# Kernel tuning notes

Measured on AMD Instinct MI355X. Metric: run time of the kernel, lower is better.

## Reference

```python
import jax, jax.numpy as jnp
import numpy as np

T = 2048        # Tmax encoder frames
EPROJS = 1024   # encoder projection dim (Henc)
DUNITS = 512    # prediction net hidden
EMBED = 512     # embedding dim
JOINT = 512     # joint space dim
ODIM = 10000    # output vocab
BLANK = 0


def setup_inputs() -> dict:
    key = jax.random.key(0)
    ks = jax.random.split(key, 11)
    def g(k, shape, scale):
        return (jax.random.normal(k, shape, dtype=jnp.float32) * scale)
    inp = {
        'h': jax.random.normal(ks[0], (T, EPROJS), dtype=jnp.float32),
        # Embedding with padding_idx=blank -> blank row zeroed
        'embed': g(ks[1], (ODIM, EMBED), 0.05).at[BLANK].set(0.0),
        # LSTMCell params (torch gate order: i, f, g, o)
        'W_ih': g(ks[2], (4 * DUNITS, EMBED), 1.0 / np.sqrt(EMBED)),
        'W_hh': g(ks[3], (4 * DUNITS, DUNITS), 1.0 / np.sqrt(DUNITS)),
        'b_ih': g(ks[4], (4 * DUNITS,), 0.01),
        'b_hh': g(ks[5], (4 * DUNITS,), 0.01),
        # joint network
        'W_enc': g(ks[6], (JOINT, EPROJS), 1.0 / np.sqrt(EPROJS)),
        'b_enc': g(ks[7], (JOINT,), 0.01),
        'W_dec': g(ks[8], (JOINT, DUNITS), 1.0 / np.sqrt(DUNITS)),  # no bias
        'W_out': g(ks[9], (ODIM, JOINT), 1.0 / np.sqrt(JOINT)),
        'b_out': g(ks[10], (ODIM,), 0.01),
    }
    return inp


def _lstm_cell(x, h_prev, c_prev, W_ih, W_hh, b_ih, b_hh):
    gates = W_ih @ x + b_ih + W_hh @ h_prev + b_hh  # (4*DUNITS,)
    i, f, g, o = jnp.split(gates, 4)
    c = jax.nn.sigmoid(f) * c_prev + jax.nn.sigmoid(i) * jnp.tanh(g)
    h = jax.nn.sigmoid(o) * jnp.tanh(c)
    return h, c


def reference(h, embed, W_ih, W_hh, b_ih, b_hh, W_enc, b_enc, W_dec, W_out, b_out):
    # Precompute encoder-side joint projection (same math, hoisted out of loop)
    h_proj = h @ W_enc.T + b_enc  # (T, JOINT)

    # Initial prediction-net step on zero embedding from zero state
    zeros_e = jnp.zeros((EMBED,), dtype=h.dtype)
    zeros_d = jnp.zeros((DUNITS,), dtype=h.dtype)
    y0, c0 = _lstm_cell(zeros_e, zeros_d, zeros_d, W_ih, W_hh, b_ih, b_hh)

    def step(carry, hp_t):
        y, c, score = carry
        # joint: tanh(lin_enc(h_t) + lin_dec(y)) -> lin_out -> log_softmax
        ytu = jax.nn.log_softmax(W_out @ jnp.tanh(hp_t + W_dec @ y) + b_out)
        logp = jnp.max(ytu)
        pred = jnp.argmax(ytu)
        emitted = pred != BLANK
        # Candidate prediction-net update with embedded token
        ey = embed[pred]
        y_new, c_new = _lstm_cell(ey, y, c, W_ih, W_hh, b_ih, b_hh)
        y = jnp.where(emitted, y_new, y)
        c = jnp.where(emitted, c_new, c)
        score = score + jnp.where(emitted, logp, jnp.zeros_like(logp))
        tok = jnp.where(emitted, pred, BLANK).astype(jnp.int32)
        return (y, c, score), tok

    (y, c, score), yseq = jax.lax.scan(step, (y0, c0, jnp.float32(0.0)), h_proj)
    # yseq: (T,) int32, BLANK where no symbol was emitted at that frame
    return yseq, score
```

## Files before the change

kernel.cpp:

```cpp
#include <hip/hip_runtime.h>
#include <stdint.h>

typedef unsigned long long u64;
typedef uint32_t u32;

#define NB     256
#define NT     256
#define TMAX   2048
#define EPROJS 1024
#define DUNITS 512
#define EMBED  512
#define JOINT  512
#define ODIM   10000

#define N_LSTM 32
#define CONS0  32
#define N_CONS 223
#define AGG_B  255
#define MAGIC  0xD07ED07Eu

#define WS_PK   0
#define WS_SA   7168
#define WS_DN   14336
#define WS_AGG  15360
#define WS_CNT  16384
#define WS_Y    17408
#define WS_U    21504
#define WS_HP   54272

__device__ __forceinline__ float aloadf(const float* p){
  return __hip_atomic_load(p, __ATOMIC_RELAXED, __HIP_MEMORY_SCOPE_AGENT);
}
__device__ __forceinline__ void astoref(float* p, float v){
  __hip_atomic_store(p, v, __ATOMIC_RELAXED, __HIP_MEMORY_SCOPE_AGENT);
}
__device__ __forceinline__ u64 aloadu64(const u64* p){
  return __hip_atomic_load(p, __ATOMIC_RELAXED, __HIP_MEMORY_SCOPE_AGENT);
}
__device__ __forceinline__ void astoreu64(u64* p, u64 v){
  __hip_atomic_store(p, v, __ATOMIC_RELAXED, __HIP_MEMORY_SCOPE_AGENT);
}
__device__ __forceinline__ u32 aloadu32(const u32* p){
  return __hip_atomic_load(p, __ATOMIC_RELAXED, __HIP_MEMORY_SCOPE_AGENT);
}
__device__ __forceinline__ void astoreu32(u32* p, u32 v){
  __hip_atomic_store(p, v, __ATOMIC_RELAXED, __HIP_MEMORY_SCOPE_AGENT);
}

__device__ __forceinline__ u32 ordbits(float f){
  u32 u = __float_as_uint(f);
  return (u & 0x80000000u) ? ~u : (u | 0x80000000u);
}
__device__ __forceinline__ float unordbits(u32 o){
  u32 u = (o & 0x80000000u) ? (o & 0x7fffffffu) : ~o;
  return __uint_as_float(u);
}
__device__ __forceinline__ float sigmoidf_(float x){ return 1.0f/(1.0f+expf(-x)); }

__device__ __forceinline__ float wredsum(float v){
  #pragma unroll
  for (int o=32;o>0;o>>=1) v += __shfl_xor(v, o);
  return v;
}
__device__ __forceinline__ u64 wredmax64(u64 v){
  #pragma unroll
  for (int o=32;o>0;o>>=1){ u64 x = __shfl_xor(v, o); v = (x>v)?x:v; }
  return v;
}

__device__ __forceinline__ int zslot(int j){
  return (j&7)*64 + ((j>>3) ^ ((j&7)<<2));
}

#define LOAD8(dst, baseptr) { const float4* _p=(const float4*)(baseptr); \
  float4 _a=_p[0], _b=_p[1]; \
  dst[0]=_a.x; dst[1]=_a.y; dst[2]=_a.z; dst[3]=_a.w; \
  dst[4]=_b.x; dst[5]=_b.y; dst[6]=_b.z; dst[7]=_b.w; }

__global__ void rnnt_init(char* ws){
  u32* p = (u32*)ws;
  const int stride = blockDim.x * gridDim.x;
  for (int i = blockIdx.x*blockDim.x + threadIdx.x; i < 13568; i += stride) p[i] = 0u;
}

__global__ void __launch_bounds__(NT, 1)
rnnt_decode(const float* __restrict__ h,    const float* __restrict__ embed,
            const float* __restrict__ W_ih, const float* __restrict__ W_hh,
            const float* __restrict__ b_ih, const float* __restrict__ b_hh,
            const float* __restrict__ W_enc,const float* __restrict__ b_enc,
            const float* __restrict__ W_dec,const float* __restrict__ W_out,
            const float* __restrict__ b_out,
            float* __restrict__ out, char* __restrict__ ws)
{
  const int b    = blockIdx.x;
  const int tid  = threadIdx.x;
  const int lane = tid & 63;
  const int w    = tid >> 6;

  u64*   ytag = (u64*)(ws + WS_Y);
  float* ubuf = (float*)(ws + WS_U);
  u64*  pkall = (u64*)(ws + WS_PK);
  u64*  saall = (u64*)(ws + WS_SA);
  u32*  done  = (u32*)(ws + WS_DN);
  u32*  aggr  = (u32*)(ws + WS_AGG);
  u32*  cnt   = (u32*)(ws + WS_CNT);
  float* hp   = (float*)(ws + WS_HP);

  __shared__ float smem[8192];
  float* PL = smem;
  float* GL = &smem[4416];
  u64*   R64= (u64*)&smem[4480];
  float* RF = &smem[4488];
  float* YO = &smem[4492];
  float* SL = &smem[4544];

  {
    float (*lds_h)[EPROJS] = (float(*)[EPROJS])smem;
    #pragma unroll
    for (int r=0;r<8;r++){
      const float4 hv = *(const float4*)(h + (size_t)(8*b + r)*EPROJS + tid*4);
      *(float4*)&lds_h[r][tid*4] = hv;
    }
    __syncthreads();
    for (int p=0;p<2;p++){
      const int j = p*NT + tid;
      float acc[8] = {0,0,0,0,0,0,0,0};
      const float4* wrow = (const float4*)(W_enc + (size_t)j*EPROJS);
      for (int k4=0;k4<EPROJS/4;k4++){
        const float4 wv = wrow[k4];
        #pragma unroll
        for (int t8=0;t8<8;t8++){
          const float4 hv = *(const float4*)&lds_h[t8][k4*4];
          acc[t8] = fmaf(wv.x,hv.x, fmaf(wv.y,hv.y, fmaf(wv.z,hv.z, fmaf(wv.w,hv.w, acc[t8]))));
        }
      }
      const float be = b_enc[j];
      #pragma unroll
      for (int t8=0;t8<8;t8++)
        astoref(&hp[(size_t)(8*b+t8)*JOINT + j], acc[t8] + be);
    }
    asm volatile("s_waitcnt vmcnt(0)" ::: "memory");
    if (tid==0) astoreu32(&done[b], MAGIC);
    __syncthreads();
  }

  if (b < N_LSTM){
    const int d = b;
    float wih[16][8], whh[16][8];
    #pragma unroll
    for (int q=0;q<16;q++){
      const int gr = w*DUNITS + 16*d + q;
      LOAD8(wih[q], W_ih + (size_t)gr*EMBED  + lane*8);
      LOAD8(whh[q], W_hh + (size_t)gr*DUNITS + lane*8);
    }
    float wdc0[16], wdc1[16];
    {
      const float4* p0 = (const float4*)(W_dec + (size_t)(2*tid)*DUNITS   + 16*d);
      const float4* p1 = (const float4*)(W_dec + (size_t)(2*tid+1)*DUNITS + 16*d);
      #pragma unroll
      for (int k4=0;k4<4;k4++){
        const float4 a = p0[k4];
        wdc0[4*k4+0]=a.x; wdc0[4*k4+1]=a.y; wdc0[4*k4+2]=a.z; wdc0[4*k4+3]=a.w;
        const float4 c = p1[k4];
        wdc1[4*k4+0]=c.x; wdc1[4*k4+1]=c.y; wdc1[4*k4+2]=c.z; wdc1[4*k4+3]=c.w;
      }
    }
    float bias_r = 0.0f;
    if (tid < 64){
      const int gr = (tid>>4)*DUNITS + 16*d + (tid&15);
      bias_r = b_ih[gr] + b_hh[gr];
    }
    float c_st = 0.0f, y_st = 0.0f;
    if (tid < 16){
      const int j = 16*d + tid;
      const float gi = b_ih[j]            + b_hh[j];
      const float gg = b_ih[2*DUNITS + j] + b_hh[2*DUNITS + j];
      const float go = b_ih[3*DUNITS + j] + b_hh[3*DUNITS + j];
      c_st = sigmoidf_(gi)*tanhf(gg);
      y_st = sigmoidf_(go)*tanhf(c_st);
      YO[tid] = y_st;
      astoreu64(&ytag[j], ((u64)1u<<32) | (u64)__float_as_uint(y_st));
    }
    __syncthreads();
    {
      float p0=0.f, p1=0.f;
      #pragma unroll
      for (int k=0;k<16;k++){ p0 = fmaf(wdc0[k], YO[k], p0); p1 = fmaf(wdc1[k], YO[k], p1); }
      float* up = ubuf + 1*4096 + (d&7)*512;
      atomicAdd(&up[2*tid],   p0);
      atomicAdd(&up[2*tid+1], p1);
    }
    asm volatile("s_waitcnt vmcnt(0)" ::: "memory");
    __syncthreads();
    if (tid < 8) atomicAdd(&cnt[tid*32], 1u);

    for (int t=0;t<TMAX;t++){
      const u32 g = (u32)(t+1);
      u64 ya, yb;
      for(;;){
        ya = aloadu64(&ytag[2*tid]); yb = aloadu64(&ytag[2*tid+1]);
        const int ok = ((u32)(ya>>32)==g) & ((u32)(yb>>32)==g);
        if (__syncthreads_and(ok)) break;
      }
      SL[zslot(2*tid)]   = __uint_as_float((u32)ya);
      SL[zslot(2*tid+1)] = __uint_as_float((u32)yb);
      __syncthreads();
      float y8[8];
      #pragma unroll
      for (int e=0;e<8;e++) y8[e] = SL[e*64 + (lane ^ (e<<2))];
      float vp[16];
      #pragma unroll
      for (int q=0;q<16;q++){
        float a=0.f;
        #pragma unroll
        for (int k=0;k<8;k++) a = fmaf(whh[q][k], y8[k], a);
        vp[q] = a;
      }
      u64 pk = 0;
      for(;;){
        if (tid < N_CONS) pk = aloadu64(&pkall[(g&3)*224 + tid]);
        const int ok = (tid < N_CONS) ? ((u32)(pk>>48) >= g) : 1;
        if (__syncthreads_and(ok)) break;
      }
      const u64 m = wredmax64(pk);
      if (lane==0) R64[w] = m;
      const int predw = (int)((~(u32)m) & 0xFFFFu);
      float e8[8];
      LOAD8(e8, embed + (size_t)predw*EMBED + 8*lane);
      __syncthreads();
      u64 best = R64[0];
      #pragma unroll
      for (int i=1;i<4;i++){ const u64 x=R64[i]; best = (x>best)?x:best; }
      const int pred = (int)((~(u32)best) & 0xFFFFu);
      const int emitted = (pred != 0);
      if (m != best){
        LOAD8(e8, embed + (size_t)pred*EMBED + 8*lane);
      }
      if (tid < 64){
        u64* uz = (u64*)(ubuf + (g&1)*4096 + (d&7)*512) + (d>>3)*64;
        astoreu64(&uz[tid], 0ull);
      }
      #pragma unroll
      for (int q=0;q<16;q++){
        float a = vp[q];
        #pragma unroll
        for (int k=0;k<8;k++) a = fmaf(wih[q][k], e8[k], a);
        PL[(w*16+q)*68 + lane] = a;
      }
      __syncthreads();
      if (tid < 64){
        const float* row = &PL[tid*68];
        float s = bias_r;
        #pragma unroll
        for (int k4=0;k4<16;k4++){
          const float4 v4 = *(const float4*)&row[4*k4];
          s += v4.x + v4.y + v4.z + v4.w;
        }
        GL[tid] = s;
      }
      __syncthreads();
      if (tid < 16){
        const float gi=GL[tid], gf=GL[16+tid], gg=GL[32+tid], go=GL[48+tid];
        const float cn = sigmoidf_(gf)*c_st + sigmoidf_(gi)*tanhf(gg);
        const float yn = sigmoidf_(go)*tanhf(cn);
        if (emitted){ c_st = cn; y_st = yn; }
        YO[tid] = y_st;
        if (t < TMAX-1)
          astoreu64(&ytag[16*d + tid], ((u64)(g+1)<<32) | (u64)__float_as_uint(y_st));
      }
      __syncthreads();
      if (t < TMAX-1){
        float p0=0.f, p1=0.f;
        #pragma unroll
        for (int k=0;k<16;k++){ p0 = fmaf(wdc0[k], YO[k], p0); p1 = fmaf(wdc1[k], YO[k], p1); }
        float* up = ubuf + ((g+1)&1)*4096 + (d&7)*512;
        atomicAdd(&up[2*tid],   p0);
        atomicAdd(&up[2*tid+1], p1);
      }
      asm volatile("s_waitcnt vmcnt(0)" ::: "memory");
      __syncthreads();
      if (t < TMAX-1 && tid < 8) atomicAdd(&cnt[tid*32], 1u);
    }
  }
  else if (b < AGG_B){
    const int cb = b - CONS0;
    int rowstart, rowcnt;
    if (cb < 188){ rowstart = cb*45;                 rowcnt = 45; }
    else         { rowstart = 8460 + (cb-188)*44;    rowcnt = 44; }
    float wout[12][8];
    #pragma unroll
    for (int q=0;q<12;q++){
      const int s = 12*w + q;
      if (s < rowcnt){
        LOAD8(wout[q], W_out + (size_t)(rowstart+s)*JOINT + lane*8);
      } else {
        #pragma unroll
        for (int k=0;k<8;k++) wout[q][k]=0.f;
      }
    }
    float my_bo = 0.f; int my_row = 0; bool my_val = false;
    if (tid < rowcnt){ my_val = true; my_row = rowstart + tid; my_bo = b_out[my_row]; }
    const u32* agrep = &aggr[(cb&7)*32];

    for(;;){
      const int ok = (aloadu32(&done[tid]) == MAGIC);
      if (__syncthreads_and(ok)) break;
    }

    const u32* cp = &cnt[(cb&7)*32];
    const int j0 = 2*tid, j1 = 2*tid+1;
    const int s0 = zslot(j0), s1 = zslot(j1);
    for (int t=0;t<TMAX;t++){
      const u32 g = (u32)(t+1);
      const float2 h2 = *(const float2*)(hp + (size_t)t*JOINT + j0);
      if (tid==0){ while (aloadu32(cp) < 32u*g) {} }
      __syncthreads();
      float u0 = 0.f, u1 = 0.f;
      {
        const u64* ub64 = (const u64*)(ubuf + (g&1)*4096) + tid;
        u64 v[8];
        #pragma unroll
        for (int r=0;r<8;r++) v[r] = aloadu64(ub64 + r*256);
        #pragma unroll
        for (int r=0;r<8;r++){
          u0 += __uint_as_float((u32)v[r]);
          u1 += __uint_as_float((u32)(v[r]>>32));
        }
      }
      SL[s0] = tanhf(h2.x + u0);
      SL[s1] = tanhf(h2.y + u1);
      __syncthreads();
      float z8[8];
      #pragma unroll
      for (int e=0;e<8;e++) z8[e] = SL[e*64 + (lane ^ (e<<2))];
      #pragma unroll
      for (int q=0;q<12;q++){
        float a=0.f;
        #pragma unroll
        for (int k=0;k<8;k++) a = fmaf(wout[q][k], z8[k], a);
        PL[(12*w+q)*68 + lane] = a;
      }
      __syncthreads();
      u64 key = 0; float lg = 0.f;
      if (tid < 48){
        const float* row = &PL[tid*68];
        float s = my_bo;
        #pragma unroll
        for (int k4=0;k4<16;k4++){
          const float4 v4 = *(const float4*)&row[4*k4];
          s += v4.x + v4.y + v4.z + v4.w;
        }
        lg = s;
        if (my_val) key = ((u64)ordbits(lg)<<16) | (u64)(0xFFFFu & ~(u32)my_row);
      }
      if (w == 0){
        const u64 bk = wredmax64(key);
        const float mw = unordbits((u32)(bk>>16));
        const float e  = my_val ? __expf(lg - mw) : 0.f;
        const float sw = wredsum(e);
        if (lane == 0){
          while ((int)(g - aloadu32(agrep)) > 3) __builtin_amdgcn_s_sleep(2);
          astoreu64(&saall[(g&3)*224 + cb], ((u64)g<<32) | (u64)__float_as_uint(sw));
          astoreu64(&pkall[(g&3)*224 + cb], ((u64)g<<48) | bk);
        }
      }
      __syncthreads();
    }
  }
  else {
    float score = 0.0f;
    for (int t=0;t<TMAX;t++){
      const u32 g = (u32)(t+1);
      const u64* pks = pkall + (g&3)*224;
      const u64* sas = saall + (g&3)*224;
      u64 pk=0, sa=0;
      for(;;){
        if (tid < N_CONS){ pk = aloadu64(&pks[tid]); sa = aloadu64(&sas[tid]); }
        const int ok = (tid < N_CONS) ? (((u32)(pk>>48)==g) & (((u32)(sa>>32))==g)) : 1;
        if (__syncthreads_and(ok)) break;
      }
      { u64 m = wredmax64(pk); if (lane==0) R64[w]=m; }
      __syncthreads();
      u64 best = R64[0];
      #pragma unroll
      for (int i=1;i<4;i++){ const u64 x=R64[i]; best = (x>best)?x:best; }
      const float mstar = unordbits((u32)(best>>16));
      float term = (tid < N_CONS) ?
        __uint_as_float((u32)sa) * __expf(unordbits((u32)(pk>>16)) - mstar) : 0.f;
      term = wredsum(term);
      if (lane==0) RF[w] = term;
      __syncthreads();
      if (tid==0){
        const float S = RF[0]+RF[1]+RF[2]+RF[3];
        const int pred = (int)((~(u32)best) & 0xFFFFu);
        if (pred != 0) score += -logf(S);
        out[t] = (float)pred;
      }
      __syncthreads();
      if (tid < 8) astoreu32(&aggr[tid*32], g);
    }
    if (tid==0) out[TMAX] = score;
  }
}

extern "C" void kernel_launch(void* const* d_in, const int* in_sizes, int n_in,
                              void* d_out, int out_size, void* d_ws, size_t ws_size,
                              hipStream_t stream)
{
  const float* h     = (const float*)d_in[0];
  const float* embed = (const float*)d_in[1];
  const float* W_ih  = (const float*)d_in[2];
  const float* W_hh  = (const float*)d_in[3];
  const float* b_ih  = (const float*)d_in[4];
  const float* b_hh  = (const float*)d_in[5];
  const float* W_enc = (const float*)d_in[6];
  const float* b_enc = (const float*)d_in[7];
  const float* W_dec = (const float*)d_in[8];
  const float* W_out = (const float*)d_in[9];
  const float* b_out = (const float*)d_in[10];
  float* out = (float*)d_out;
  char* ws = (char*)d_ws;

  hipLaunchKernelGGL(rnnt_init, dim3(32), dim3(NT), 0, stream, ws);
  hipLaunchKernelGGL(rnnt_decode, dim3(NB), dim3(NT), 0, stream,
                     h, embed, W_ih, W_hh, b_ih, b_hh, W_enc, b_enc, W_dec, W_out, b_out,
                     out, ws);
}
```

Before: 16.71 ms.

## Replace LDS partial-sum reductions with wave shuffles and per-block done flags

Both the LSTM blocks and the joint-output consumer blocks now reduce their dot-product partials with in-wave shuffle sums instead of writing to shared memory and doing a second serial pass. The shared counter that the LSTM blocks incremented atomically is replaced by a per-block generation flag, which consumers poll in parallel with a block-wide vote. The aggregator back-pressure load is also issued early. This is meant to shorten the per-timestep critical path on the serial decode chain, at the cost of more shuffle instructions and wider polling traffic.

```diff
diff --git a/kernel.cpp b/kernel.cpp
--- a/kernel.cpp
+++ b/kernel.cpp
@@ -23,10 +23,10 @@
 #define WS_SA   7168
 #define WS_DN   14336
 #define WS_AGG  15360
-#define WS_CNT  16384
-#define WS_Y    17408
-#define WS_U    21504
-#define WS_HP   54272
+#define WS_UD   16384
+#define WS_Y    20480
+#define WS_U    24576
+#define WS_HP   57344
 
 __device__ __forceinline__ float aloadf(const float* p){
   return __hip_atomic_load(p, __ATOMIC_RELAXED, __HIP_MEMORY_SCOPE_AGENT);
@@ -80,7 +80,7 @@
 __global__ void rnnt_init(char* ws){
   u32* p = (u32*)ws;
   const int stride = blockDim.x * gridDim.x;
-  for (int i = blockIdx.x*blockDim.x + threadIdx.x; i < 13568; i += stride) p[i] = 0u;
+  for (int i = blockIdx.x*blockDim.x + threadIdx.x; i < 14336; i += stride) p[i] = 0u;
 }
 
 __global__ void __launch_bounds__(NT, 1)
@@ -103,11 +103,10 @@
   u64*  saall = (u64*)(ws + WS_SA);
   u32*  done  = (u32*)(ws + WS_DN);
   u32*  aggr  = (u32*)(ws + WS_AGG);
-  u32*  cnt   = (u32*)(ws + WS_CNT);
+  u32*  udone = (u32*)(ws + WS_UD);
   float* hp   = (float*)(ws + WS_HP);
 
   __shared__ float smem[8192];
-  float* PL = smem;
   float* GL = &smem[4416];
   u64*   R64= (u64*)&smem[4480];
   float* RF = &smem[4488];
@@ -165,10 +164,10 @@
         wdc1[4*k4+0]=c.x; wdc1[4*k4+1]=c.y; wdc1[4*k4+2]=c.z; wdc1[4*k4+3]=c.w;
       }
     }
-    float bias_r = 0.0f;
-    if (tid < 64){
-      const int gr = (tid>>4)*DUNITS + 16*d + (tid&15);
-      bias_r = b_ih[gr] + b_hh[gr];
+    float bias_l = 0.0f;
+    if (lane < 16){
+      const int gr = w*DUNITS + 16*d + lane;
+      bias_l = b_ih[gr] + b_hh[gr];
     }
     float c_st = 0.0f, y_st = 0.0f;
     if (tid < 16){
@@ -192,7 +191,7 @@
     }
     asm volatile("s_waitcnt vmcnt(0)" ::: "memory");
     __syncthreads();
-    if (tid < 8) atomicAdd(&cnt[tid*32], 1u);
+    if (tid==0) astoreu32(&udone[d*32], 1u);
 
     for (int t=0;t<TMAX;t++){
       const u32 g = (u32)(t+1);
@@ -240,23 +239,22 @@
         u64* uz = (u64*)(ubuf + (g&1)*4096 + (d&7)*512) + (d>>3)*64;
         astoreu64(&uz[tid], 0ull);
       }
-      #pragma unroll
-      for (int q=0;q<16;q++){
-        float a = vp[q];
-        #pragma unroll
-        for (int k=0;k<8;k++) a = fmaf(wih[q][k], e8[k], a);
-        PL[(w*16+q)*68 + lane] = a;
-      }
-      __syncthreads();
-      if (tid < 64){
-        const float* row = &PL[tid*68];
-        float s = bias_r;
-        #pragma unroll
-        for (int k4=0;k4<16;k4++){
-          const float4 v4 = *(const float4*)&row[4*k4];
-          s += v4.x + v4.y + v4.z + v4.w;
-        }
-        GL[tid] = s;
+      {
+        float a[16];
+        #pragma unroll
+        for (int q=0;q<16;q++){
+          float acc = vp[q];
+          #pragma unroll
+          for (int k=0;k<8;k++) acc = fmaf(wih[q][k], e8[k], acc);
+          a[q] = acc;
+        }
+        float rs = 0.f;
+        #pragma unroll
+        for (int q=0;q<16;q++){
+          const float s = wredsum(a[q]);
+          if (lane==q) rs = s;
+        }
+        if (lane < 16) GL[w*16 + lane] = rs + bias_l;
       }
       __syncthreads();
       if (tid < 16){
@@ -279,7 +277,7 @@
       }
       asm volatile("s_waitcnt vmcnt(0)" ::: "memory");
       __syncthreads();
-      if (t < TMAX-1 && tid < 8) atomicAdd(&cnt[tid*32], 1u);
+      if (t < TMAX-1 && tid==0) astoreu32(&udone[d*32], g+1);
     }
   }
   else if (b < AGG_B){
@@ -298,8 +296,10 @@
         for (int k=0;k<8;k++) wout[q][k]=0.f;
       }
     }
-    float my_bo = 0.f; int my_row = 0; bool my_val = false;
-    if (tid < rowcnt){ my_val = true; my_row = rowstart + tid; my_bo = b_out[my_row]; }
+    const int s12 = 12*w + lane;
+    const bool my_val = (lane < 12) && (s12 < rowcnt);
+    const int my_row = rowstart + s12;
+    const float my_bo = my_val ? b_out[my_row] : 0.f;
     const u32* agrep = &aggr[(cb&7)*32];
 
     for(;;){
@@ -307,14 +307,15 @@
       if (__syncthreads_and(ok)) break;
     }
 
-    const u32* cp = &cnt[(cb&7)*32];
     const int j0 = 2*tid, j1 = 2*tid+1;
     const int s0 = zslot(j0), s1 = zslot(j1);
     for (int t=0;t<TMAX;t++){
       const u32 g = (u32)(t+1);
       const float2 h2 = *(const float2*)(hp + (size_t)t*JOINT + j0);
-      if (tid==0){ while (aloadu32(cp) < 32u*g) {} }
-      __syncthreads();
+      for(;;){
+        const u32 dv = (tid < N_LSTM) ? aloadu32(&udone[tid*32]) : g;
+        if (__syncthreads_and(dv >= g)) break;
+      }
       float u0 = 0.f, u1 = 0.f;
       {
         const u64* ub64 = (const u64*)(ubuf + (g&1)*4096) + tid;
@@ -327,42 +328,49 @@
           u1 += __uint_as_float((u32)(v[r]>>32));
         }
       }
+      u32 agv = 0;
+      if (tid==0) agv = aloadu32(agrep);
       SL[s0] = tanhf(h2.x + u0);
       SL[s1] = tanhf(h2.y + u1);
       __syncthreads();
       float z8[8];
       #pragma unroll
       for (int e=0;e<8;e++) z8[e] = SL[e*64 + (lane ^ (e<<2))];
-      #pragma unroll
-      for (int q=0;q<12;q++){
-        float a=0.f;
-        #pragma unroll
-        for (int k=0;k<8;k++) a = fmaf(wout[q][k], z8[k], a);
-        PL[(12*w+q)*68 + lane] = a;
-      }
-      __syncthreads();
-      u64 key = 0; float lg = 0.f;
-      if (tid < 48){
-        const float* row = &PL[tid*68];
-        float s = my_bo;
-        #pragma unroll
-        for (int k4=0;k4<16;k4++){
-          const float4 v4 = *(const float4*)&row[4*k4];
-          s += v4.x + v4.y + v4.z + v4.w;
-        }
-        lg = s;
-        if (my_val) key = ((u64)ordbits(lg)<<16) | (u64)(0xFFFFu & ~(u32)my_row);
-      }
-      if (w == 0){
-        const u64 bk = wredmax64(key);
-        const float mw = unordbits((u32)(bk>>16));
-        const float e  = my_val ? __expf(lg - mw) : 0.f;
-        const float sw = wredsum(e);
-        if (lane == 0){
-          while ((int)(g - aloadu32(agrep)) > 3) __builtin_amdgcn_s_sleep(2);
-          astoreu64(&saall[(g&3)*224 + cb], ((u64)g<<32) | (u64)__float_as_uint(sw));
-          astoreu64(&pkall[(g&3)*224 + cb], ((u64)g<<48) | bk);
-        }
+      float lg = 0.f;
+      {
+        float a[12];
+        #pragma unroll
+        for (int q=0;q<12;q++){
+          float acc=0.f;
+          #pragma unroll
+          for (int k=0;k<8;k++) acc = fmaf(wout[q][k], z8[k], acc);
+          a[q] = acc;
+        }
+        float rs = 0.f;
+        #pragma unroll
+        for (int q=0;q<12;q++){
+          const float s = wredsum(a[q]);
+          if (lane==q) rs = s;
+        }
+        lg = rs + my_bo;
+      }
+      u64 key = my_val ? (((u64)ordbits(lg)<<16) | (u64)(0xFFFFu & ~(u32)my_row)) : 0;
+      const u64 kw = wredmax64(key);
+      if (lane==0) R64[w] = kw;
+      __syncthreads();
+      u64 best = R64[0];
+      #pragma unroll
+      for (int i=1;i<4;i++){ const u64 x=R64[i]; best = (x>best)?x:best; }
+      const float mw = unordbits((u32)(best>>16));
+      const float e = my_val ? __expf(lg - mw) : 0.f;
+      const float sw = wredsum(e);
+      if (lane==0) RF[w] = sw;
+      __syncthreads();
+      if (tid==0){
+        const float S = RF[0]+RF[1]+RF[2]+RF[3];
+        while ((int)(g - agv) > 3){ __builtin_amdgcn_s_sleep(2); agv = aloadu32(agrep); }
+        astoreu64(&saall[(g&3)*224 + cb], ((u64)g<<32) | (u64)__float_as_uint(S));
+        astoreu64(&pkall[(g&3)*224 + cb], ((u64)g<<48) | best);
       }
       __syncthreads();
     }
```

Measured after the change: 21.78 ms. 1.3x slower.

## Replace atomic-add decoder projection with tagged partials and dedicated reducer blocks

Applied to the files above, without the earlier changes.

Each LSTM block now writes its W_dec·y partial sums as generation-tagged 64-bit stores into a per-block slot. Previously these were atomicAdds into a double-buffered accumulator guarded by a counter, with a full vmcnt wait and a zeroing pass. Eight new reducer blocks poll the tagged partials, sum them and publish tagged totals that the joint blocks poll directly. This removes atomic contention, the counter handshake and the buffer clearing from the recurrent critical path. In exchange the number of output-projection blocks drops from 223 to 215 (more rows per block), and a reduction hop is added between the LSTM and joint stages.

```diff
diff --git a/kernel.cpp b/kernel.cpp
--- a/kernel.cpp
+++ b/kernel.cpp
@@ -15,7 +15,8 @@
 
 #define N_LSTM 32
 #define CONS0  32
-#define N_CONS 223
+#define N_CONS 215
+#define RED0   247
 #define AGG_B  255
 #define MAGIC  0xD07ED07Eu
 
@@ -23,10 +24,10 @@
 #define WS_SA   7168
 #define WS_DN   14336
 #define WS_AGG  15360
-#define WS_CNT  16384
-#define WS_Y    17408
-#define WS_U    21504
-#define WS_HP   54272
+#define WS_Y    16384
+#define WS_U    20480
+#define WS_PART 24576
+#define WS_HP   155648
 
 __device__ __forceinline__ float aloadf(const float* p){
   return __hip_atomic_load(p, __ATOMIC_RELAXED, __HIP_MEMORY_SCOPE_AGENT);
@@ -80,7 +81,7 @@
 __global__ void rnnt_init(char* ws){
   u32* p = (u32*)ws;
   const int stride = blockDim.x * gridDim.x;
-  for (int i = blockIdx.x*blockDim.x + threadIdx.x; i < 13568; i += stride) p[i] = 0u;
+  for (int i = blockIdx.x*blockDim.x + threadIdx.x; i < 38912; i += stride) p[i] = 0u;
 }
 
 __global__ void __launch_bounds__(NT, 1)
@@ -98,16 +99,17 @@
   const int w    = tid >> 6;
 
   u64*   ytag = (u64*)(ws + WS_Y);
-  float* ubuf = (float*)(ws + WS_U);
+  u64*   utag = (u64*)(ws + WS_U);
+  u64*   ptag = (u64*)(ws + WS_PART);
   u64*  pkall = (u64*)(ws + WS_PK);
   u64*  saall = (u64*)(ws + WS_SA);
   u32*  done  = (u32*)(ws + WS_DN);
   u32*  aggr  = (u32*)(ws + WS_AGG);
-  u32*  cnt   = (u32*)(ws + WS_CNT);
   float* hp   = (float*)(ws + WS_HP);
 
   __shared__ float smem[8192];
   float* PL = smem;
+  float* PS = smem;
   float* GL = &smem[4416];
   u64*   R64= (u64*)&smem[4480];
   float* RF = &smem[4488];
@@ -186,13 +188,10 @@
       float p0=0.f, p1=0.f;
       #pragma unroll
       for (int k=0;k<16;k++){ p0 = fmaf(wdc0[k], YO[k], p0); p1 = fmaf(wdc1[k], YO[k], p1); }
-      float* up = ubuf + 1*4096 + (d&7)*512;
-      atomicAdd(&up[2*tid],   p0);
-      atomicAdd(&up[2*tid+1], p1);
-    }
-    asm volatile("s_waitcnt vmcnt(0)" ::: "memory");
-    __syncthreads();
-    if (tid < 8) atomicAdd(&cnt[tid*32], 1u);
+      u64* up = ptag + (size_t)d*512;
+      astoreu64(&up[2*tid],   ((u64)1u<<32) | (u64)__float_as_uint(p0));
+      astoreu64(&up[2*tid+1], ((u64)1u<<32) | (u64)__float_as_uint(p1));
+    }
 
     for (int t=0;t<TMAX;t++){
       const u32 g = (u32)(t+1);
@@ -235,10 +234,6 @@
       const int emitted = (pred != 0);
       if (m != best){
         LOAD8(e8, embed + (size_t)pred*EMBED + 8*lane);
-      }
-      if (tid < 64){
-        u64* uz = (u64*)(ubuf + (g&1)*4096 + (d&7)*512) + (d>>3)*64;
-        astoreu64(&uz[tid], 0ull);
       }
       #pragma unroll
       for (int q=0;q<16;q++){
@@ -273,20 +268,17 @@
         float p0=0.f, p1=0.f;
         #pragma unroll
         for (int k=0;k<16;k++){ p0 = fmaf(wdc0[k], YO[k], p0); p1 = fmaf(wdc1[k], YO[k], p1); }
-        float* up = ubuf + ((g+1)&1)*4096 + (d&7)*512;
-        atomicAdd(&up[2*tid],   p0);
-        atomicAdd(&up[2*tid+1], p1);
-      }
-      asm volatile("s_waitcnt vmcnt(0)" ::: "memory");
-      __syncthreads();
-      if (t < TMAX-1 && tid < 8) atomicAdd(&cnt[tid*32], 1u);
+        u64* up = ptag + (size_t)d*512;
+        astoreu64(&up[2*tid],   ((u64)(g+1)<<32) | (u64)__float_as_uint(p0));
+        astoreu64(&up[2*tid+1], ((u64)(g+1)<<32) | (u64)__float_as_uint(p1));
+      }
     }
   }
-  else if (b < AGG_B){
+  else if (b < RED0){
     const int cb = b - CONS0;
     int rowstart, rowcnt;
-    if (cb < 188){ rowstart = cb*45;                 rowcnt = 45; }
-    else         { rowstart = 8460 + (cb-188)*44;    rowcnt = 44; }
+    if (cb < 110){ rowstart = cb*47;                 rowcnt = 47; }
+    else         { rowstart = 5170 + (cb-110)*46;    rowcnt = 46; }
     float wout[12][8];
     #pragma unroll
     for (int q=0;q<12;q++){
@@ -307,28 +299,22 @@
       if (__syncthreads_and(ok)) break;
     }
 
-    const u32* cp = &cnt[(cb&7)*32];
     const int j0 = 2*tid, j1 = 2*tid+1;
     const int s0 = zslot(j0), s1 = zslot(j1);
     for (int t=0;t<TMAX;t++){
       const u32 g = (u32)(t+1);
       const float2 h2 = *(const float2*)(hp + (size_t)t*JOINT + j0);
-      if (tid==0){ while (aloadu32(cp) < 32u*g) {} }
-      __syncthreads();
-      float u0 = 0.f, u1 = 0.f;
-      {
-        const u64* ub64 = (const u64*)(ubuf + (g&1)*4096) + tid;
-        u64 v[8];
-        #pragma unroll
-        for (int r=0;r<8;r++) v[r] = aloadu64(ub64 + r*256);
-        #pragma unroll
-        for (int r=0;r<8;r++){
-          u0 += __uint_as_float((u32)v[r]);
-          u1 += __uint_as_float((u32)(v[r]>>32));
-        }
-      }
-      SL[s0] = tanhf(h2.x + u0);
-      SL[s1] = tanhf(h2.y + u1);
+      u64 ua, ub2;
+      for(;;){
+        ua  = aloadu64(&utag[j0]);
+        ub2 = aloadu64(&utag[j1]);
+        const int ok = (((u32)(ua>>32))>=g) & (((u32)(ub2>>32))>=g);
+        if (__syncthreads_and(ok)) break;
+      }
+      u32 agv = 0;
+      if (tid==0) agv = aloadu32(agrep);
+      SL[s0] = tanhf(h2.x + __uint_as_float((u32)ua));
+      SL[s1] = tanhf(h2.y + __uint_as_float((u32)ub2));
       __syncthreads();
       float z8[8];
       #pragma unroll
@@ -359,12 +345,38 @@
         const float e  = my_val ? __expf(lg - mw) : 0.f;
         const float sw = wredsum(e);
         if (lane == 0){
-          while ((int)(g - aloadu32(agrep)) > 3) __builtin_amdgcn_s_sleep(2);
+          while ((int)(g - agv) > 3){ __builtin_amdgcn_s_sleep(2); agv = aloadu32(agrep); }
           astoreu64(&saall[(g&3)*224 + cb], ((u64)g<<32) | (u64)__float_as_uint(sw));
           astoreu64(&pkall[(g&3)*224 + cb], ((u64)g<<48) | bk);
         }
       }
       __syncthreads();
+    }
+  }
+  else if (b < AGG_B){
+    const int rr = b - RED0;
+    const int ebase = 64*rr;
+    for (int t=0;t<TMAX;t++){
+      const u32 g = (u32)(t+1);
+      u64 pv[8];
+      for(;;){
+        bool ok = true;
+        #pragma unroll
+        for (int i=0;i<8;i++){
+          pv[i] = aloadu64(&ptag[(size_t)(8*w+i)*512 + ebase + lane]);
+          ok &= ((u32)(pv[i]>>32) >= g);
+        }
+        if (__syncthreads_and(ok)) break;
+      }
+      float s = 0.f;
+      #pragma unroll
+      for (int i=0;i<8;i++) s += __uint_as_float((u32)pv[i]);
+      PS[w*64 + lane] = s;
+      __syncthreads();
+      if (tid < 64){
+        const float tot = PS[tid] + PS[64+tid] + PS[128+tid] + PS[192+tid];
+        astoreu64(&utag[ebase + tid], ((u64)g<<32) | (u64)__float_as_uint(tot));
+      }
     }
   }
   else {
```

New measurement: 18.49 ms. +10.7%, slower.
